# Kernel tuning notes

Hardware: AMD Instinct MI355X
Metric: run time of the kernel (lower is better)

Reference implementation:

```python
import jax, jax.numpy as jnp
import numpy as np

N_NODES = 50000
N_EDGES = 800000
IN_DIM = 256
HIDDEN = 32
HEADS = 4
OUT_DIM = 64


def setup_inputs() -> dict:
    key = jax.random.key(0)
    k1, k2, k3, k4, k5, k6, k7 = jax.random.split(key, 7)
    h = jax.random.normal(k1, (N_NODES, IN_DIM), dtype=jnp.float32)
    src = jax.random.randint(k2, (N_EDGES,), 0, N_NODES, dtype=jnp.int32)
    dst = jax.random.randint(k3, (N_EDGES,), 0, N_NODES, dtype=jnp.int32)
    # xavier_normal with relu gain, per-head weights
    gain = float(np.sqrt(2.0))
    W1 = gain * jnp.sqrt(2.0 / (IN_DIM + HIDDEN)) * jax.random.normal(k4, (HEADS, IN_DIM, HIDDEN), dtype=jnp.float32)
    a1 = gain * jnp.sqrt(2.0 / (2 * HIDDEN + 1)) * jax.random.normal(k5, (HEADS, 2 * HIDDEN), dtype=jnp.float32)
    W2 = gain * jnp.sqrt(2.0 / (HIDDEN * HEADS + OUT_DIM)) * jax.random.normal(k6, (1, HIDDEN * HEADS, OUT_DIM), dtype=jnp.float32)
    a2 = gain * jnp.sqrt(2.0 / (2 * OUT_DIM + 1)) * jax.random.normal(k7, (1, 2 * OUT_DIM), dtype=jnp.float32)
    return {"h": h, "src": src, "dst": dst, "W1": W1, "a1": a1, "W2": W2, "a2": a2}


def _gat_layer(x, src, dst, W, a):
    # x: [N, in], W: [H, in, d], a: [H, 2d]
    N = x.shape[0]
    d = W.shape[-1]
    z = jnp.einsum('ni,hio->nho', x, W)                    # [N, H, d]
    a_s, a_d = a[:, :d], a[:, d:]
    es = jnp.einsum('nho,ho->nh', z, a_s)                  # per-node src score
    ed = jnp.einsum('nho,ho->nh', z, a_d)                  # per-node dst score
    e = jax.nn.leaky_relu(es[src] + ed[dst])               # [E, H]
    # segment (per-destination) softmax over incoming edges
    emax = jax.ops.segment_max(e, dst, num_segments=N)     # [N, H]
    ex = jnp.exp(e - emax[dst])
    denom = jax.ops.segment_sum(ex, dst, num_segments=N)   # [N, H]
    alpha = ex / denom[dst]                                # [E, H]
    # scatter weighted sum of source feats back to destinations
    out = jax.ops.segment_sum(alpha[:, :, None] * z[src], dst, num_segments=N)  # [N, H, d]
    return out.reshape(N, -1)


def reference(h, src, dst, W1, a1, W2, a2):
    h1 = jax.nn.elu(_gat_layer(h, src, dst, W1, a1))       # [N, HEADS*HIDDEN]
    return _gat_layer(h1, src, dst, W2, a2)                # [N, OUT_DIM]
```

## Files before the change

kernel.cpp:

```cpp
#include <hip/hip_runtime.h>
#include <hip/hip_bf16.h>
#include <math.h>

#define N_NODES 50000
#define N_EDGES 800000
#define IN_DIM 256
#define HID 32
#define HEADS 4
#define OUT_DIM 64

#define SCAN_CHUNK 1024
#define SCAN_BLOCKS ((N_NODES + SCAN_CHUNK - 1) / SCAN_CHUNK)

typedef __attribute__((ext_vector_type(8))) short bf16x8;
typedef __attribute__((ext_vector_type(4))) float f32x4;

__device__ __forceinline__ float lrelu(float e) { return e > 0.f ? e : 0.01f * e; }
__device__ __forceinline__ float bflo(unsigned u) { return __uint_as_float(u << 16); }
__device__ __forceinline__ float bfhi(unsigned u) { return __uint_as_float(u & 0xffff0000u); }

__device__ __forceinline__ unsigned short rne_bf16(float x) {
    unsigned u = __float_as_uint(x);
    unsigned r = u + 0x7fffu + ((u >> 16) & 1u);
    return (unsigned short)(r >> 16);
}

__device__ __forceinline__ void splitf(float x, short& hi, short& lo) {
    unsigned u = __float_as_uint(x);
    unsigned short h = (unsigned short)(u >> 16);
    float hf = __uint_as_float(((unsigned)h) << 16);
    float l = x - hf;
    unsigned short lb = (unsigned short)(__float_as_uint(l) >> 16);
    hi = (short)h;
    lo = (short)lb;
}


__global__ void __launch_bounds__(256) prep_kernel(
        const float* __restrict__ W1, const float* __restrict__ a1,
        const float* __restrict__ W2, const float* __restrict__ a2,
        unsigned short* __restrict__ B1h, unsigned short* __restrict__ B1l,
        unsigned short* __restrict__ B2h, unsigned short* __restrict__ B2l,
        int* __restrict__ count) {
    int gid = blockIdx.x * 256 + threadIdx.x;
    if (gid < N_NODES) count[gid] = 0;

    int k = blockIdx.x;
    int c = threadIdx.x;
    if (c < 144) {
        float val = 0.f;
        if (c < 128) {
            val = W1[(size_t)(c >> 5) * IN_DIM * HID + (size_t)k * HID + (c & 31)];
        } else if (c < 136) {
            int j = c - 128;
            int hd = (j < 4) ? j : (j - 4);
            int off = (j < 4) ? 0 : HID;
            const float* Wp = W1 + (size_t)hd * IN_DIM * HID + (size_t)k * HID;
            const float* ap = a1 + hd * 2 * HID + off;
            float s = 0.f;
            for (int o = 0; o < HID; o++) s += Wp[o] * ap[o];
            val = s;
        }
        unsigned short hi = rne_bf16(val);
        float hf = __uint_as_float(((unsigned)hi) << 16);
        unsigned short lo = rne_bf16(val - hf);
        int s_ = k >> 5, q = (k >> 3) & 3, j8 = k & 7;
        int nt = c >> 4, L = q * 16 + (c & 15);
        size_t idx = (((size_t)s_ * 9 + nt) * 64 + L) * 8 + j8;
        B1h[idx] = hi;
        B1l[idx] = lo;
    } else if (c >= 160 && c < 240 && k < 128) {
        int c2 = c - 160;
        float val = 0.f;
        if (c2 < 64) {
            val = W2[(size_t)k * OUT_DIM + c2];
        } else if (c2 < 66) {
            const float* ap = a2 + (c2 - 64) * OUT_DIM;
            const float* Wp = W2 + (size_t)k * OUT_DIM;
            float s = 0.f;
            for (int o = 0; o < OUT_DIM; o++) s += Wp[o] * ap[o];
            val = s;
        }
        unsigned short hi = rne_bf16(val);
        float hf = __uint_as_float(((unsigned)hi) << 16);
        unsigned short lo = rne_bf16(val - hf);
        int s_ = k >> 5, q = (k >> 3) & 3, j8 = k & 7;
        int nt = c2 >> 4, L = q * 16 + (c2 & 15);
        size_t idx = (((size_t)s_ * 5 + nt) * 64 + L) * 8 + j8;
        B2h[idx] = hi;
        B2l[idx] = lo;
    }
}


__global__ void hist_kernel(const int* __restrict__ dst, int* __restrict__ count,
                            int* __restrict__ rank) {
    int i = blockIdx.x * blockDim.x + threadIdx.x;
    if (i < N_EDGES) rank[i] = atomicAdd(&count[dst[i]], 1);
}

__global__ void scan1_kernel(const int* __restrict__ count, int* __restrict__ row_start,
                             int* __restrict__ blocksum) {
    __shared__ int sdata[256];
    int t = threadIdx.x;
    int base = blockIdx.x * SCAN_CHUNK + t * 4;
    int v[4];
    int s = 0;
#pragma unroll
    for (int j = 0; j < 4; j++) {
        int idx = base + j;
        int x = (idx < N_NODES) ? count[idx] : 0;
        v[j] = x;
        s += x;
    }
    sdata[t] = s;
    __syncthreads();
    for (int off = 1; off < 256; off <<= 1) {
        int u = (t >= off) ? sdata[t - off] : 0;
        __syncthreads();
        sdata[t] += u;
        __syncthreads();
    }
    int excl = sdata[t] - s;
#pragma unroll
    for (int j = 0; j < 4; j++) {
        int idx = base + j;
        if (idx < N_NODES) row_start[idx] = excl;
        excl += v[j];
    }
    if (t == 255) blocksum[blockIdx.x] = sdata[255];
}

__global__ void scan23_kernel(int* __restrict__ row_start, const int* __restrict__ blocksum) {
    __shared__ int pre;
    int t = threadIdx.x;
    if (t < 64) {
        int v = (t < SCAN_BLOCKS) ? blocksum[t] : 0;
#pragma unroll
        for (int off = 1; off < 64; off <<= 1) {
            int u = __shfl_up(v, off);
            if (t >= off) v += u;
        }
        if (t == blockIdx.x) pre = v - blocksum[t];
    }
    __syncthreads();
    int add = pre;
    int base = blockIdx.x * SCAN_CHUNK + t * 4;
#pragma unroll
    for (int j = 0; j < 4; j++) {
        int idx = base + j;
        if (idx < N_NODES) row_start[idx] += add;
    }
}

__global__ void scatter_kernel(const int* __restrict__ src, const int* __restrict__ dst,
                               const int* __restrict__ rank, const int* __restrict__ row_start,
                               int* __restrict__ esrc) {
    int i = blockIdx.x * blockDim.x + threadIdx.x;
    if (i < N_EDGES) esrc[row_start[dst[i]] + rank[i]] = src[i];
}


__global__ void __launch_bounds__(256) proj1_mfma(
        const float* __restrict__ h, const unsigned short* __restrict__ Bh,
        const unsigned short* __restrict__ Bl, __hip_bfloat16* __restrict__ z1b,
        float* __restrict__ es1, float* __restrict__ ed1) {
    int tid = threadIdx.x;
    int wave = tid >> 6;
    int L = tid & 63;
    int q = L >> 4, L15 = L & 15;
    int n0 = blockIdx.x * 64 + wave * 16;

    int rowA = n0 + L15;
    int rrA = rowA < N_NODES ? rowA : N_NODES - 1;
    const float* hrow = h + (size_t)rrA * IN_DIM + q * 8;

    f32x4 acc[9];
#pragma unroll
    for (int nt = 0; nt < 9; nt++) acc[nt] = (f32x4)(0.f);

    float4 x0 = *(const float4*)(hrow);
    float4 x1 = *(const float4*)(hrow + 4);

#pragma unroll
    for (int s = 0; s < 8; s++) {
        int sn = (s < 7) ? s + 1 : 7;
        float4 p0 = *(const float4*)(hrow + sn * 32);
        float4 p1 = *(const float4*)(hrow + sn * 32 + 4);

        float xs[8] = {x0.x, x0.y, x0.z, x0.w, x1.x, x1.y, x1.z, x1.w};
        bf16x8 ah, al;
#pragma unroll
        for (int j = 0; j < 8; j++) {
            short hi, lo;
            splitf(xs[j], hi, lo);
            ah[j] = hi;
            al[j] = lo;
        }

        const bf16x8* bhp = (const bf16x8*)(Bh + ((size_t)s * 9 * 64) * 8 + (size_t)L * 8);
        const bf16x8* blp = (const bf16x8*)(Bl + ((size_t)s * 9 * 64) * 8 + (size_t)L * 8);
#pragma unroll
        for (int nt = 0; nt < 9; nt++) {
            bf16x8 bh = bhp[nt * 64];
            acc[nt] = __builtin_amdgcn_mfma_f32_16x16x32_bf16(ah, bh, acc[nt], 0, 0, 0);
            acc[nt] = __builtin_amdgcn_mfma_f32_16x16x32_bf16(al, bh, acc[nt], 0, 0, 0);
        }
        {
            bf16x8 bl8 = blp[8 * 64];
            acc[8] = __builtin_amdgcn_mfma_f32_16x16x32_bf16(ah, bl8, acc[8], 0, 0, 0);
        }
        x0 = p0;
        x1 = p1;
    }

#pragma unroll
    for (int r = 0; r < 4; r++) {
        int rowc = n0 + q * 4 + r;
        if (rowc < N_NODES) {
#pragma unroll
            for (int nt = 0; nt < 8; nt++)
                z1b[(size_t)rowc * 128 + nt * 16 + L15] = __float2bfloat16(acc[nt][r]);
            if (L15 < 4) es1[rowc * HEADS + L15] = acc[8][r];
            else if (L15 < 8) ed1[rowc * HEADS + (L15 - 4)] = acc[8][r];
        }
    }
}


__global__ void __launch_bounds__(256) agg1_kernel(
        const __hip_bfloat16* __restrict__ z1b, const float* __restrict__ es1,
        const float* __restrict__ ed1, const int* __restrict__ row_start,
        const int* __restrict__ count, const int* __restrict__ esrc,
        __hip_bfloat16* __restrict__ h1b) {
    int v = blockIdx.x * 4 + (threadIdx.x >> 6);
    int L = threadIdx.x & 63;
    int sub = L >> 4;
    int c16 = L & 15;
    int hd = c16 >> 2;
    int beg = row_start[v], deg = count[v];
    float edv = ed1[v * HEADS + hd];
    const int* ep = esrc + beg;
    float lacc = 0.f;
    float acc[8];
#pragma unroll
    for (int i = 0; i < 8; i++) acc[i] = 0.f;
    const uint4* zq = (const uint4*)z1b;

    for (int j0 = 0; j0 < deg; j0 += 32) {
        int se[8];
        uint4 u[8];
        float ev[8];
#pragma unroll
        for (int g = 0; g < 8; g++) {
            if (j0 + g * 4 < deg) {
                int e = j0 + g * 4 + sub;
                se[g] = ep[(e < deg) ? e : 0];
            }
        }
#pragma unroll
        for (int g = 0; g < 8; g++) {
            if (j0 + g * 4 < deg) {
                u[g] = zq[(size_t)se[g] * 16 + c16];
                ev[g] = es1[se[g] * HEADS + hd];
            }
        }
#pragma unroll
        for (int g = 0; g < 8; g++) {
            if (j0 + g * 4 < deg) {
                bool val = (j0 + g * 4 + sub) < deg;
                float q = val ? __expf(lrelu(ev[g] + edv)) : 0.f;
                lacc += q;
                acc[0] = fmaf(q, bflo(u[g].x), acc[0]);
                acc[1] = fmaf(q, bfhi(u[g].x), acc[1]);
                acc[2] = fmaf(q, bflo(u[g].y), acc[2]);
                acc[3] = fmaf(q, bfhi(u[g].y), acc[3]);
                acc[4] = fmaf(q, bflo(u[g].z), acc[4]);
                acc[5] = fmaf(q, bfhi(u[g].z), acc[5]);
                acc[6] = fmaf(q, bflo(u[g].w), acc[6]);
                acc[7] = fmaf(q, bfhi(u[g].w), acc[7]);
            }
        }
    }
    lacc += __shfl_xor(lacc, 1);
    lacc += __shfl_xor(lacc, 2);
    lacc += __shfl_xor(lacc, 16);
    lacc += __shfl_xor(lacc, 32);
    lacc *= 0.25f;
#pragma unroll
    for (int i = 0; i < 8; i++) {
        acc[i] += __shfl_xor(acc[i], 16);
        acc[i] += __shfl_xor(acc[i], 32);
    }
    if (L < 16) {
        float inv = (deg > 0) ? 1.f / lacc : 0.f;
        unsigned w[4];
#pragma unroll
        for (int i = 0; i < 4; i++) {
            float r0 = acc[2 * i] * inv;
            float r1 = acc[2 * i + 1] * inv;
            r0 = r0 > 0.f ? r0 : __expf(r0) - 1.f;
            r1 = r1 > 0.f ? r1 : __expf(r1) - 1.f;
            w[i] = (unsigned)rne_bf16(r0) | ((unsigned)rne_bf16(r1) << 16);
        }
        uint4* dst = (uint4*)(h1b + (size_t)v * 128 + c16 * 8);
        *dst = make_uint4(w[0], w[1], w[2], w[3]);
    }
}


__global__ void __launch_bounds__(256) proj2_mfma(
        const __hip_bfloat16* __restrict__ h1b, const unsigned short* __restrict__ Bh,
        const unsigned short* __restrict__ Bl, __hip_bfloat16* __restrict__ z2b,
        float* __restrict__ es2, float* __restrict__ ed2) {
    int tid = threadIdx.x;
    int wave = tid >> 6;
    int L = tid & 63;
    int q = L >> 4, L15 = L & 15;
    int n0 = blockIdx.x * 64 + wave * 16;

    int rowA = n0 + L15;
    int rrA = rowA < N_NODES ? rowA : N_NODES - 1;
    const bf16x8* hq = (const bf16x8*)(h1b + (size_t)rrA * 128);

    f32x4 acc[5];
#pragma unroll
    for (int nt = 0; nt < 5; nt++) acc[nt] = (f32x4)(0.f);

#pragma unroll
    for (int s = 0; s < 4; s++) {
        bf16x8 a = hq[s * 4 + q];
        const bf16x8* bhp = (const bf16x8*)(Bh + ((size_t)s * 5 * 64) * 8 + (size_t)L * 8);
        const bf16x8* blp = (const bf16x8*)(Bl + ((size_t)s * 5 * 64) * 8 + (size_t)L * 8);
#pragma unroll
        for (int nt = 0; nt < 5; nt++)
            acc[nt] = __builtin_amdgcn_mfma_f32_16x16x32_bf16(a, bhp[nt * 64], acc[nt], 0, 0, 0);
        acc[4] = __builtin_amdgcn_mfma_f32_16x16x32_bf16(a, blp[4 * 64], acc[4], 0, 0, 0);
    }

#pragma unroll
    for (int r = 0; r < 4; r++) {
        int rowc = n0 + q * 4 + r;
        if (rowc < N_NODES) {
#pragma unroll
            for (int nt = 0; nt < 4; nt++)
                z2b[(size_t)rowc * OUT_DIM + nt * 16 + L15] = __float2bfloat16(acc[nt][r]);
            if (L15 == 0) es2[rowc] = acc[4][r];
            else if (L15 == 1) ed2[rowc] = acc[4][r];
        }
    }
}


__global__ void __launch_bounds__(256) agg2_kernel(
        const __hip_bfloat16* __restrict__ z2b, const float* __restrict__ es2,
        const float* __restrict__ ed2, const int* __restrict__ row_start,
        const int* __restrict__ count, const int* __restrict__ esrc,
        float* __restrict__ out) {
    int v = blockIdx.x * 4 + (threadIdx.x >> 6);
    int L = threadIdx.x & 63;
    int sub = L >> 3;
    int c8 = L & 7;
    int beg = row_start[v], deg = count[v];
    float edv = ed2[v];
    const int* ep = esrc + beg;
    float lacc = 0.f;
    float acc[8];
#pragma unroll
    for (int i = 0; i < 8; i++) acc[i] = 0.f;
    const uint4* zq = (const uint4*)z2b;

    for (int j0 = 0; j0 < deg; j0 += 32) {
        int se[4];
        uint4 u[4];
        float ev[4];
#pragma unroll
        for (int g = 0; g < 4; g++) {
            if (j0 + g * 8 < deg) {
                int e = j0 + g * 8 + sub;
                se[g] = ep[(e < deg) ? e : 0];
            }
        }
#pragma unroll
        for (int g = 0; g < 4; g++) {
            if (j0 + g * 8 < deg) {
                u[g] = zq[(size_t)se[g] * 8 + c8];
                ev[g] = es2[se[g]];
            }
        }
#pragma unroll
        for (int g = 0; g < 4; g++) {
            if (j0 + g * 8 < deg) {
                bool val = (j0 + g * 8 + sub) < deg;
                float q = val ? __expf(lrelu(ev[g] + edv)) : 0.f;
                lacc += q;
                acc[0] = fmaf(q, bflo(u[g].x), acc[0]);
                acc[1] = fmaf(q, bfhi(u[g].x), acc[1]);
                acc[2] = fmaf(q, bflo(u[g].y), acc[2]);
                acc[3] = fmaf(q, bfhi(u[g].y), acc[3]);
                acc[4] = fmaf(q, bflo(u[g].z), acc[4]);
                acc[5] = fmaf(q, bfhi(u[g].z), acc[5]);
                acc[6] = fmaf(q, bflo(u[g].w), acc[6]);
                acc[7] = fmaf(q, bfhi(u[g].w), acc[7]);
            }
        }
    }
    lacc += __shfl_xor(lacc, 8);
    lacc += __shfl_xor(lacc, 16);
    lacc += __shfl_xor(lacc, 32);
#pragma unroll
    for (int i = 0; i < 8; i++) {
        acc[i] += __shfl_xor(acc[i], 8);
        acc[i] += __shfl_xor(acc[i], 16);
        acc[i] += __shfl_xor(acc[i], 32);
    }
    if (L < 8) {
        float inv = (deg > 0) ? 1.f / lacc : 0.f;
        float4 r0, r1;
#pragma unroll
        for (int i = 0; i < 8; i++) {
            float r = acc[i] * inv;
            if (i < 4) (&r0.x)[i] = r;
            else (&r1.x)[i - 4] = r;
        }
        float* dst = out + (size_t)v * OUT_DIM + c8 * 8;
        *(float4*)dst = r0;
        *(float4*)(dst + 4) = r1;
    }
}


extern "C" void kernel_launch(void* const* d_in, const int* in_sizes, int n_in,
                              void* d_out, int out_size, void* d_ws, size_t ws_size,
                              hipStream_t stream) {
    const float* h  = (const float*)d_in[0];
    const int* src  = (const int*)d_in[1];
    const int* dst  = (const int*)d_in[2];
    const float* W1 = (const float*)d_in[3];
    const float* a1 = (const float*)d_in[4];
    const float* W2 = (const float*)d_in[5];
    const float* a2 = (const float*)d_in[6];
    float* out = (float*)d_out;

    char* w = (char*)d_ws;
    size_t off = 0;
    auto alloc = [&](size_t bytes) {
        void* p = w + off;
        off = (off + bytes + 255) & ~(size_t)255;
        return p;
    };
    __hip_bfloat16* z1b = (__hip_bfloat16*)alloc((size_t)N_NODES * 128 * 2);
    float* es1 = (float*)alloc((size_t)N_NODES * HEADS * 4);
    float* ed1 = (float*)alloc((size_t)N_NODES * HEADS * 4);
    __hip_bfloat16* h1b = (__hip_bfloat16*)alloc((size_t)N_NODES * 128 * 2);
    __hip_bfloat16* z2b = (__hip_bfloat16*)alloc((size_t)N_NODES * OUT_DIM * 2);
    float* es2 = (float*)alloc((size_t)N_NODES * 4);
    float* ed2 = (float*)alloc((size_t)N_NODES * 4);
    int* count     = (int*)alloc((size_t)N_NODES * 4);
    int* row_start = (int*)alloc((size_t)N_NODES * 4);
    int* rank      = (int*)alloc((size_t)N_EDGES * 4);
    int* blocksum  = (int*)alloc((size_t)SCAN_BLOCKS * 4);
    int* esrc      = (int*)alloc((size_t)N_EDGES * 4);
    unsigned short* Bf1h = (unsigned short*)alloc((size_t)8 * 9 * 64 * 8 * 2);
    unsigned short* Bf1l = (unsigned short*)alloc((size_t)8 * 9 * 64 * 8 * 2);
    unsigned short* Bf2h = (unsigned short*)alloc((size_t)4 * 5 * 64 * 8 * 2);
    unsigned short* Bf2l = (unsigned short*)alloc((size_t)4 * 5 * 64 * 8 * 2);

    prep_kernel<<<256, 256, 0, stream>>>(W1, a1, W2, a2, Bf1h, Bf1l, Bf2h, Bf2l, count);
    hist_kernel<<<(N_EDGES + 255) / 256, 256, 0, stream>>>(dst, count, rank);
    scan1_kernel<<<SCAN_BLOCKS, 256, 0, stream>>>(count, row_start, blocksum);
    scan23_kernel<<<SCAN_BLOCKS, 256, 0, stream>>>(row_start, blocksum);
    scatter_kernel<<<(N_EDGES + 255) / 256, 256, 0, stream>>>(src, dst, rank, row_start, esrc);

    const int MBLK = (N_NODES + 63) / 64;
    proj1_mfma<<<MBLK, 256, 0, stream>>>(h, Bf1h, Bf1l, z1b, es1, ed1);
    agg1_kernel<<<N_NODES / 4, 256, 0, stream>>>(z1b, es1, ed1, row_start, count, esrc, h1b);
    proj2_mfma<<<MBLK, 256, 0, stream>>>(h1b, Bf2h, Bf2l, z2b, es2, ed2);
    agg2_kernel<<<N_NODES / 4, 256, 0, stream>>>(z2b, es2, ed2, row_start, count, esrc, out);
}
```

Baseline: 234.4 us.

## Fuse CSR build and layer-1 projection into one cooperative kernel

Replaces the six front-end launches (prep, histogram, two scans, scatter, proj1) with a single cooperative kernel. Half the blocks build the CSR using software grid barriers and keep dst and rank in registers, so the rank array is no longer written and reread. The other half prepare weights and then run the layer-1 MFMA projection concurrently. This removes launch gaps and overlaps the latency-bound CSR work with the compute-bound projection, at the cost of spin-wait barriers, a memset, and a fallback path if the cooperative launch fails.

```diff
diff --git a/kernel.cpp b/kernel.cpp
--- a/kernel.cpp
+++ b/kernel.cpp
@@ -11,6 +11,13 @@
 
 #define SCAN_CHUNK 1024
 #define SCAN_BLOCKS ((N_NODES + SCAN_CHUNK - 1) / SCAN_CHUNK)
+
+#define NCSR 512
+#define NPROJ 512
+#define NGRID (NCSR + NPROJ)
+#define CSR_T (NCSR * 256)
+#define EPT ((N_EDGES + CSR_T - 1) / CSR_T)
+#define NTASK ((N_NODES + 15) / 16)
 
 typedef __attribute__((ext_vector_type(8))) short bf16x8;
 typedef __attribute__((ext_vector_type(4))) float f32x4;
@@ -36,17 +43,25 @@
 }
 
 
-__global__ void __launch_bounds__(256) prep_kernel(
+__device__ __forceinline__ void bar_wait(int* ctr, int nblk) {
+    __syncthreads();
+    if (threadIdx.x == 0) {
+        __threadfence();
+        __hip_atomic_fetch_add(ctr, 1, __ATOMIC_RELEASE, __HIP_MEMORY_SCOPE_AGENT);
+        while (__hip_atomic_load(ctr, __ATOMIC_RELAXED, __HIP_MEMORY_SCOPE_AGENT) < nblk) {
+            __builtin_amdgcn_s_sleep(8);
+        }
+        __threadfence();
+    }
+    __syncthreads();
+}
+
+
+__device__ __forceinline__ void prep_body(int k, int c,
         const float* __restrict__ W1, const float* __restrict__ a1,
         const float* __restrict__ W2, const float* __restrict__ a2,
         unsigned short* __restrict__ B1h, unsigned short* __restrict__ B1l,
-        unsigned short* __restrict__ B2h, unsigned short* __restrict__ B2l,
-        int* __restrict__ count) {
-    int gid = blockIdx.x * 256 + threadIdx.x;
-    if (gid < N_NODES) count[gid] = 0;
-
-    int k = blockIdx.x;
-    int c = threadIdx.x;
+        unsigned short* __restrict__ B2h, unsigned short* __restrict__ B2l) {
     if (c < 144) {
         float val = 0.f;
         if (c < 128) {
@@ -92,18 +107,9 @@
     }
 }
 
-
-__global__ void hist_kernel(const int* __restrict__ dst, int* __restrict__ count,
-                            int* __restrict__ rank) {
-    int i = blockIdx.x * blockDim.x + threadIdx.x;
-    if (i < N_EDGES) rank[i] = atomicAdd(&count[dst[i]], 1);
-}
-
-__global__ void scan1_kernel(const int* __restrict__ count, int* __restrict__ row_start,
-                             int* __restrict__ blocksum) {
-    __shared__ int sdata[256];
-    int t = threadIdx.x;
-    int base = blockIdx.x * SCAN_CHUNK + t * 4;
+__device__ __forceinline__ void scan1_body(int bid, int t, const int* __restrict__ count,
+        int* __restrict__ row_start, int* __restrict__ blocksum, int* sdata) {
+    int base = bid * SCAN_CHUNK + t * 4;
     int v[4];
     int s = 0;
 #pragma unroll
@@ -128,12 +134,11 @@
         if (idx < N_NODES) row_start[idx] = excl;
         excl += v[j];
     }
-    if (t == 255) blocksum[blockIdx.x] = sdata[255];
-}
-
-__global__ void scan23_kernel(int* __restrict__ row_start, const int* __restrict__ blocksum) {
-    __shared__ int pre;
-    int t = threadIdx.x;
+    if (t == 255) blocksum[bid] = sdata[255];
+}
+
+__device__ __forceinline__ void scan23_body(int bid, int t, int* __restrict__ row_start,
+        const int* __restrict__ blocksum, int* pre) {
     if (t < 64) {
         int v = (t < SCAN_BLOCKS) ? blocksum[t] : 0;
 #pragma unroll
@@ -141,16 +146,156 @@
             int u = __shfl_up(v, off);
             if (t >= off) v += u;
         }
-        if (t == blockIdx.x) pre = v - blocksum[t];
+        if (t == bid) *pre = v - blocksum[t];
     }
     __syncthreads();
-    int add = pre;
-    int base = blockIdx.x * SCAN_CHUNK + t * 4;
+    int add = *pre;
+    int base = bid * SCAN_CHUNK + t * 4;
 #pragma unroll
     for (int j = 0; j < 4; j++) {
         int idx = base + j;
         if (idx < N_NODES) row_start[idx] += add;
     }
+}
+
+__device__ __forceinline__ void proj1_body(int n0, int L,
+        const float* __restrict__ h, const unsigned short* __restrict__ Bh,
+        const unsigned short* __restrict__ Bl, __hip_bfloat16* __restrict__ z1b,
+        float* __restrict__ es1, float* __restrict__ ed1) {
+    int q = L >> 4, L15 = L & 15;
+    int rowA = n0 + L15;
+    int rrA = rowA < N_NODES ? rowA : N_NODES - 1;
+    const float* hrow = h + (size_t)rrA * IN_DIM + q * 8;
+
+    f32x4 acc[9];
+#pragma unroll
+    for (int nt = 0; nt < 9; nt++) acc[nt] = (f32x4)(0.f);
+
+    float4 x0 = *(const float4*)(hrow);
+    float4 x1 = *(const float4*)(hrow + 4);
+
+#pragma unroll
+    for (int s = 0; s < 8; s++) {
+        int sn = (s < 7) ? s + 1 : 7;
+        float4 p0 = *(const float4*)(hrow + sn * 32);
+        float4 p1 = *(const float4*)(hrow + sn * 32 + 4);
+
+        float xs[8] = {x0.x, x0.y, x0.z, x0.w, x1.x, x1.y, x1.z, x1.w};
+        bf16x8 ah, al;
+#pragma unroll
+        for (int j = 0; j < 8; j++) {
+            short hi, lo;
+            splitf(xs[j], hi, lo);
+            ah[j] = hi;
+            al[j] = lo;
+        }
+
+        const bf16x8* bhp = (const bf16x8*)(Bh + ((size_t)s * 9 * 64) * 8 + (size_t)L * 8);
+        const bf16x8* blp = (const bf16x8*)(Bl + ((size_t)s * 9 * 64) * 8 + (size_t)L * 8);
+#pragma unroll
+        for (int nt = 0; nt < 9; nt++) {
+            bf16x8 bh = bhp[nt * 64];
+            acc[nt] = __builtin_amdgcn_mfma_f32_16x16x32_bf16(ah, bh, acc[nt], 0, 0, 0);
+            acc[nt] = __builtin_amdgcn_mfma_f32_16x16x32_bf16(al, bh, acc[nt], 0, 0, 0);
+        }
+        {
+            bf16x8 bl8 = blp[8 * 64];
+            acc[8] = __builtin_amdgcn_mfma_f32_16x16x32_bf16(ah, bl8, acc[8], 0, 0, 0);
+        }
+        x0 = p0;
+        x1 = p1;
+    }
+
+#pragma unroll
+    for (int r = 0; r < 4; r++) {
+        int rowc = n0 + q * 4 + r;
+        if (rowc < N_NODES) {
+#pragma unroll
+            for (int nt = 0; nt < 8; nt++)
+                z1b[(size_t)rowc * 128 + nt * 16 + L15] = __float2bfloat16(acc[nt][r]);
+            if (L15 < 4) es1[rowc * HEADS + L15] = acc[8][r];
+            else if (L15 < 8) ed1[rowc * HEADS + (L15 - 4)] = acc[8][r];
+        }
+    }
+}
+
+
+__global__ void __launch_bounds__(256, 4) fused_front(
+        const float* __restrict__ h, const float* __restrict__ W1,
+        const float* __restrict__ a1, const float* __restrict__ W2,
+        const float* __restrict__ a2,
+        unsigned short* __restrict__ B1h, unsigned short* __restrict__ B1l,
+        unsigned short* __restrict__ B2h, unsigned short* __restrict__ B2l,
+        const int* __restrict__ src, const int* __restrict__ dst,
+        int* __restrict__ count, int* __restrict__ row_start,
+        int* __restrict__ blocksum, int* __restrict__ esrc,
+        __hip_bfloat16* __restrict__ z1b, float* __restrict__ es1,
+        float* __restrict__ ed1, int* __restrict__ bars) {
+    __shared__ int sdata[256];
+    __shared__ int pre;
+    int bid = blockIdx.x;
+    int t = threadIdx.x;
+
+    if (bid < NCSR) {
+        int gid = bid * 256 + t;
+        if (gid < N_NODES) atomicExch(&count[gid], 0);
+        bar_wait(&bars[0], NCSR);
+        int dv[EPT], rv[EPT];
+#pragma unroll
+        for (int k = 0; k < EPT; k++) {
+            int e = gid + k * CSR_T;
+            if (e < N_EDGES) {
+                dv[k] = dst[e];
+                rv[k] = atomicAdd(&count[dv[k]], 1);
+            }
+        }
+        bar_wait(&bars[1], NCSR);
+        if (bid < SCAN_BLOCKS) scan1_body(bid, t, count, row_start, blocksum, sdata);
+        bar_wait(&bars[2], NCSR);
+        if (bid < SCAN_BLOCKS) scan23_body(bid, t, row_start, blocksum, &pre);
+        bar_wait(&bars[3], NCSR);
+#pragma unroll
+        for (int k = 0; k < EPT; k++) {
+            int e = gid + k * CSR_T;
+            if (e < N_EDGES) esrc[row_start[dv[k]] + rv[k]] = src[e];
+        }
+    } else {
+        int k = bid - NCSR;
+        if (k < 256) prep_body(k, t, W1, a1, W2, a2, B1h, B1l, B2h, B2l);
+        bar_wait(&bars[4], NPROJ);
+        int wave = t >> 6, L = t & 63;
+        for (int task = k * 4 + wave; task < NTASK; task += NPROJ * 4)
+            proj1_body(task * 16, L, h, B1h, B1l, z1b, es1, ed1);
+    }
+}
+
+
+__global__ void __launch_bounds__(256) prep_kernel(
+        const float* __restrict__ W1, const float* __restrict__ a1,
+        const float* __restrict__ W2, const float* __restrict__ a2,
+        unsigned short* __restrict__ B1h, unsigned short* __restrict__ B1l,
+        unsigned short* __restrict__ B2h, unsigned short* __restrict__ B2l,
+        int* __restrict__ count) {
+    int gid = blockIdx.x * 256 + threadIdx.x;
+    if (gid < N_NODES) count[gid] = 0;
+    prep_body(blockIdx.x, threadIdx.x, W1, a1, W2, a2, B1h, B1l, B2h, B2l);
+}
+
+__global__ void hist_kernel(const int* __restrict__ dst, int* __restrict__ count,
+                            int* __restrict__ rank) {
+    int i = blockIdx.x * blockDim.x + threadIdx.x;
+    if (i < N_EDGES) rank[i] = atomicAdd(&count[dst[i]], 1);
+}
+
+__global__ void scan1_kernel(const int* __restrict__ count, int* __restrict__ row_start,
+                             int* __restrict__ blocksum) {
+    __shared__ int sdata[256];
+    scan1_body(blockIdx.x, threadIdx.x, count, row_start, blocksum, sdata);
+}
+
+__global__ void scan23_kernel(int* __restrict__ row_start, const int* __restrict__ blocksum) {
+    __shared__ int pre;
+    scan23_body(blockIdx.x, threadIdx.x, row_start, blocksum, &pre);
 }
 
 __global__ void scatter_kernel(const int* __restrict__ src, const int* __restrict__ dst,
@@ -159,7 +304,6 @@
     int i = blockIdx.x * blockDim.x + threadIdx.x;
     if (i < N_EDGES) esrc[row_start[dst[i]] + rank[i]] = src[i];
 }
-
 
 __global__ void __launch_bounds__(256) proj1_mfma(
         const float* __restrict__ h, const unsigned short* __restrict__ Bh,
@@ -168,63 +312,8 @@
     int tid = threadIdx.x;
     int wave = tid >> 6;
     int L = tid & 63;
-    int q = L >> 4, L15 = L & 15;
     int n0 = blockIdx.x * 64 + wave * 16;
-
-    int rowA = n0 + L15;
-    int rrA = rowA < N_NODES ? rowA : N_NODES - 1;
-    const float* hrow = h + (size_t)rrA * IN_DIM + q * 8;
-
-    f32x4 acc[9];
-#pragma unroll
-    for (int nt = 0; nt < 9; nt++) acc[nt] = (f32x4)(0.f);
-
-    float4 x0 = *(const float4*)(hrow);
-    float4 x1 = *(const float4*)(hrow + 4);
-
-#pragma unroll
-    for (int s = 0; s < 8; s++) {
-        int sn = (s < 7) ? s + 1 : 7;
-        float4 p0 = *(const float4*)(hrow + sn * 32);
-        float4 p1 = *(const float4*)(hrow + sn * 32 + 4);
-
-        float xs[8] = {x0.x, x0.y, x0.z, x0.w, x1.x, x1.y, x1.z, x1.w};
-        bf16x8 ah, al;
-#pragma unroll
-        for (int j = 0; j < 8; j++) {
-            short hi, lo;
-            splitf(xs[j], hi, lo);
-            ah[j] = hi;
-            al[j] = lo;
-        }
-
-        const bf16x8* bhp = (const bf16x8*)(Bh + ((size_t)s * 9 * 64) * 8 + (size_t)L * 8);
-        const bf16x8* blp = (const bf16x8*)(Bl + ((size_t)s * 9 * 64) * 8 + (size_t)L * 8);
-#pragma unroll
-        for (int nt = 0; nt < 9; nt++) {
-            bf16x8 bh = bhp[nt * 64];
-            acc[nt] = __builtin_amdgcn_mfma_f32_16x16x32_bf16(ah, bh, acc[nt], 0, 0, 0);
-            acc[nt] = __builtin_amdgcn_mfma_f32_16x16x32_bf16(al, bh, acc[nt], 0, 0, 0);
-        }
-        {
-            bf16x8 bl8 = blp[8 * 64];
-            acc[8] = __builtin_amdgcn_mfma_f32_16x16x32_bf16(ah, bl8, acc[8], 0, 0, 0);
-        }
-        x0 = p0;
-        x1 = p1;
-    }
-
-#pragma unroll
-    for (int r = 0; r < 4; r++) {
-        int rowc = n0 + q * 4 + r;
-        if (rowc < N_NODES) {
-#pragma unroll
-            for (int nt = 0; nt < 8; nt++)
-                z1b[(size_t)rowc * 128 + nt * 16 + L15] = __float2bfloat16(acc[nt][r]);
-            if (L15 < 4) es1[rowc * HEADS + L15] = acc[8][r];
-            else if (L15 < 8) ed1[rowc * HEADS + (L15 - 4)] = acc[8][r];
-        }
-    }
+    proj1_body(n0, L, h, Bh, Bl, z1b, es1, ed1);
 }
 
 
@@ -303,8 +392,8 @@
             r1 = r1 > 0.f ? r1 : __expf(r1) - 1.f;
             w[i] = (unsigned)rne_bf16(r0) | ((unsigned)rne_bf16(r1) << 16);
         }
-        uint4* dst = (uint4*)(h1b + (size_t)v * 128 + c16 * 8);
-        *dst = make_uint4(w[0], w[1], w[2], w[3]);
+        uint4* dstp = (uint4*)(h1b + (size_t)v * 128 + c16 * 8);
+        *dstp = make_uint4(w[0], w[1], w[2], w[3]);
     }
 }
 
@@ -423,9 +512,9 @@
             if (i < 4) (&r0.x)[i] = r;
             else (&r1.x)[i - 4] = r;
         }
-        float* dst = out + (size_t)v * OUT_DIM + c8 * 8;
-        *(float4*)dst = r0;
-        *(float4*)(dst + 4) = r1;
+        float* dstp = out + (size_t)v * OUT_DIM + c8 * 8;
+        *(float4*)dstp = r0;
+        *(float4*)(dstp + 4) = r1;
     }
 }
 
@@ -465,15 +554,29 @@
     unsigned short* Bf1l = (unsigned short*)alloc((size_t)8 * 9 * 64 * 8 * 2);
     unsigned short* Bf2h = (unsigned short*)alloc((size_t)4 * 5 * 64 * 8 * 2);
     unsigned short* Bf2l = (unsigned short*)alloc((size_t)4 * 5 * 64 * 8 * 2);
-
-    prep_kernel<<<256, 256, 0, stream>>>(W1, a1, W2, a2, Bf1h, Bf1l, Bf2h, Bf2l, count);
-    hist_kernel<<<(N_EDGES + 255) / 256, 256, 0, stream>>>(dst, count, rank);
-    scan1_kernel<<<SCAN_BLOCKS, 256, 0, stream>>>(count, row_start, blocksum);
-    scan23_kernel<<<SCAN_BLOCKS, 256, 0, stream>>>(row_start, blocksum);
-    scatter_kernel<<<(N_EDGES + 255) / 256, 256, 0, stream>>>(src, dst, rank, row_start, esrc);
+    int* bars = (int*)alloc(8 * sizeof(int));
 
     const int MBLK = (N_NODES + 63) / 64;
-    proj1_mfma<<<MBLK, 256, 0, stream>>>(h, Bf1h, Bf1l, z1b, es1, ed1);
+
+    hipMemsetAsync(bars, 0, 8 * sizeof(int), stream);
+
+    void* kargs[] = {(void*)&h, (void*)&W1, (void*)&a1, (void*)&W2, (void*)&a2,
+                     (void*)&Bf1h, (void*)&Bf1l, (void*)&Bf2h, (void*)&Bf2l,
+                     (void*)&src, (void*)&dst, (void*)&count, (void*)&row_start,
+                     (void*)&blocksum, (void*)&esrc, (void*)&z1b, (void*)&es1,
+                     (void*)&ed1, (void*)&bars};
+    hipError_t ce = hipLaunchCooperativeKernel(
+        reinterpret_cast<const void*>(&fused_front), dim3(NGRID), dim3(256),
+        kargs, 0, stream);
+    if (ce != hipSuccess) {
+        prep_kernel<<<256, 256, 0, stream>>>(W1, a1, W2, a2, Bf1h, Bf1l, Bf2h, Bf2l, count);
+        hist_kernel<<<(N_EDGES + 255) / 256, 256, 0, stream>>>(dst, count, rank);
+        scan1_kernel<<<SCAN_BLOCKS, 256, 0, stream>>>(count, row_start, blocksum);
+        scan23_kernel<<<SCAN_BLOCKS, 256, 0, stream>>>(row_start, blocksum);
+        scatter_kernel<<<(N_EDGES + 255) / 256, 256, 0, stream>>>(src, dst, rank, row_start, esrc);
+        proj1_mfma<<<MBLK, 256, 0, stream>>>(h, Bf1h, Bf1l, z1b, es1, ed1);
+    }
+
     agg1_kernel<<<N_NODES / 4, 256, 0, stream>>>(z1b, es1, ed1, row_start, count, esrc, h1b);
     proj2_mfma<<<MBLK, 256, 0, stream>>>(h1b, Bf2h, Bf2l, z2b, es2, ed2);
     agg2_kernel<<<N_NODES / 4, 256, 0, stream>>>(z2b, es2, ed2, row_start, count, esrc, out);
```

After: 629.3 us. 168% more time.

## Fuse prep with histogram and single-block scan with proj1 to cut launches

Applied to the files above, without the earlier changes.

Merges the weight prep kernel and the edge histogram into one launch, replaces the three-kernel multi-block scan with a single-block scan, and runs that scan as block 0 of the layer-1 projection kernel. Count zeroing moves to a memset. The goal is fewer kernel launches and dependency bubbles, and letting the scan overlap with the projection. The cost is a serial scan in one block where each thread loops over about 196 strided elements with uncoalesced loads, which may end up on the critical path before scatter.

```diff
diff --git a/kernel.cpp b/kernel.cpp
--- a/kernel.cpp
+++ b/kernel.cpp
@@ -9,8 +9,8 @@
 #define HEADS 4
 #define OUT_DIM 64
 
-#define SCAN_CHUNK 1024
-#define SCAN_BLOCKS ((N_NODES + SCAN_CHUNK - 1) / SCAN_CHUNK)
+#define HIST_BLOCKS ((N_EDGES + 255) / 256)
+#define MBLK ((N_NODES + 63) / 64)
 
 typedef __attribute__((ext_vector_type(8))) short bf16x8;
 typedef __attribute__((ext_vector_type(4))) float f32x4;
@@ -36,17 +36,11 @@
 }
 
 
-__global__ void __launch_bounds__(256) prep_kernel(
+__device__ __forceinline__ void prep_body(int k, int c,
         const float* __restrict__ W1, const float* __restrict__ a1,
         const float* __restrict__ W2, const float* __restrict__ a2,
         unsigned short* __restrict__ B1h, unsigned short* __restrict__ B1l,
-        unsigned short* __restrict__ B2h, unsigned short* __restrict__ B2l,
-        int* __restrict__ count) {
-    int gid = blockIdx.x * 256 + threadIdx.x;
-    if (gid < N_NODES) count[gid] = 0;
-
-    int k = blockIdx.x;
-    int c = threadIdx.x;
+        unsigned short* __restrict__ B2h, unsigned short* __restrict__ B2l) {
     if (c < 144) {
         float val = 0.f;
         if (c < 128) {
@@ -93,25 +87,32 @@
 }
 
 
-__global__ void hist_kernel(const int* __restrict__ dst, int* __restrict__ count,
-                            int* __restrict__ rank) {
-    int i = blockIdx.x * blockDim.x + threadIdx.x;
-    if (i < N_EDGES) rank[i] = atomicAdd(&count[dst[i]], 1);
-}
-
-__global__ void scan1_kernel(const int* __restrict__ count, int* __restrict__ row_start,
-                             int* __restrict__ blocksum) {
+__global__ void __launch_bounds__(256) prep_hist_kernel(
+        const float* __restrict__ W1, const float* __restrict__ a1,
+        const float* __restrict__ W2, const float* __restrict__ a2,
+        unsigned short* __restrict__ B1h, unsigned short* __restrict__ B1l,
+        unsigned short* __restrict__ B2h, unsigned short* __restrict__ B2l,
+        const int* __restrict__ dst, int* __restrict__ count,
+        int* __restrict__ rank) {
+    int bid = blockIdx.x;
+    if (bid < 256) {
+        prep_body(bid, threadIdx.x, W1, a1, W2, a2, B1h, B1l, B2h, B2l);
+    } else {
+        int i = (bid - 256) * 256 + threadIdx.x;
+        if (i < N_EDGES) rank[i] = atomicAdd(&count[dst[i]], 1);
+    }
+}
+
+
+__device__ __forceinline__ void scan_block_body(const int* __restrict__ count,
+                                                int* __restrict__ row_start, int t) {
     __shared__ int sdata[256];
-    int t = threadIdx.x;
-    int base = blockIdx.x * SCAN_CHUNK + t * 4;
-    int v[4];
+    const int PER = (N_NODES + 255) / 256;
+    int base = t * PER;
     int s = 0;
-#pragma unroll
-    for (int j = 0; j < 4; j++) {
+    for (int j = 0; j < PER; j++) {
         int idx = base + j;
-        int x = (idx < N_NODES) ? count[idx] : 0;
-        v[j] = x;
-        s += x;
+        if (idx < N_NODES) s += count[idx];
     }
     sdata[t] = s;
     __syncthreads();
@@ -122,109 +123,99 @@
         __syncthreads();
     }
     int excl = sdata[t] - s;
-#pragma unroll
-    for (int j = 0; j < 4; j++) {
+    for (int j = 0; j < PER; j++) {
         int idx = base + j;
-        if (idx < N_NODES) row_start[idx] = excl;
-        excl += v[j];
-    }
-    if (t == 255) blocksum[blockIdx.x] = sdata[255];
-}
-
-__global__ void scan23_kernel(int* __restrict__ row_start, const int* __restrict__ blocksum) {
-    __shared__ int pre;
-    int t = threadIdx.x;
-    if (t < 64) {
-        int v = (t < SCAN_BLOCKS) ? blocksum[t] : 0;
-#pragma unroll
-        for (int off = 1; off < 64; off <<= 1) {
-            int u = __shfl_up(v, off);
-            if (t >= off) v += u;
-        }
-        if (t == blockIdx.x) pre = v - blocksum[t];
-    }
-    __syncthreads();
-    int add = pre;
-    int base = blockIdx.x * SCAN_CHUNK + t * 4;
-#pragma unroll
-    for (int j = 0; j < 4; j++) {
-        int idx = base + j;
-        if (idx < N_NODES) row_start[idx] += add;
-    }
-}
+        if (idx < N_NODES) {
+            row_start[idx] = excl;
+            excl += count[idx];
+        }
+    }
+}
+
+
+__device__ __forceinline__ void proj1_body(int n0, int L,
+        const float* __restrict__ h, const unsigned short* __restrict__ Bh,
+        const unsigned short* __restrict__ Bl, __hip_bfloat16* __restrict__ z1b,
+        float* __restrict__ es1, float* __restrict__ ed1) {
+    int q = L >> 4, L15 = L & 15;
+    int rowA = n0 + L15;
+    int rrA = rowA < N_NODES ? rowA : N_NODES - 1;
+    const float* hrow = h + (size_t)rrA * IN_DIM + q * 8;
+
+    f32x4 acc[9];
+#pragma unroll
+    for (int nt = 0; nt < 9; nt++) acc[nt] = (f32x4)(0.f);
+
+    float4 x0 = *(const float4*)(hrow);
+    float4 x1 = *(const float4*)(hrow + 4);
+
+#pragma unroll
+    for (int s = 0; s < 8; s++) {
+        int sn = (s < 7) ? s + 1 : 7;
+        float4 p0 = *(const float4*)(hrow + sn * 32);
+        float4 p1 = *(const float4*)(hrow + sn * 32 + 4);
+
+        float xs[8] = {x0.x, x0.y, x0.z, x0.w, x1.x, x1.y, x1.z, x1.w};
+        bf16x8 ah, al;
+#pragma unroll
+        for (int j = 0; j < 8; j++) {
+            short hi, lo;
+            splitf(xs[j], hi, lo);
+            ah[j] = hi;
+            al[j] = lo;
+        }
+
+        const bf16x8* bhp = (const bf16x8*)(Bh + ((size_t)s * 9 * 64) * 8 + (size_t)L * 8);
+        const bf16x8* blp = (const bf16x8*)(Bl + ((size_t)s * 9 * 64) * 8 + (size_t)L * 8);
+#pragma unroll
+        for (int nt = 0; nt < 9; nt++) {
+            bf16x8 bh = bhp[nt * 64];
+            acc[nt] = __builtin_amdgcn_mfma_f32_16x16x32_bf16(ah, bh, acc[nt], 0, 0, 0);
+            acc[nt] = __builtin_amdgcn_mfma_f32_16x16x32_bf16(al, bh, acc[nt], 0, 0, 0);
+        }
+        {
+            bf16x8 bl8 = blp[8 * 64];
+            acc[8] = __builtin_amdgcn_mfma_f32_16x16x32_bf16(ah, bl8, acc[8], 0, 0, 0);
+        }
+        x0 = p0;
+        x1 = p1;
+    }
+
+#pragma unroll
+    for (int r = 0; r < 4; r++) {
+        int rowc = n0 + q * 4 + r;
+        if (rowc < N_NODES) {
+#pragma unroll
+            for (int nt = 0; nt < 8; nt++)
+                z1b[(size_t)rowc * 128 + nt * 16 + L15] = __float2bfloat16(acc[nt][r]);
+            if (L15 < 4) es1[rowc * HEADS + L15] = acc[8][r];
+            else if (L15 < 8) ed1[rowc * HEADS + (L15 - 4)] = acc[8][r];
+        }
+    }
+}
+
+
+__global__ void __launch_bounds__(256) scan_proj1_kernel(
+        const float* __restrict__ h, const unsigned short* __restrict__ Bh,
+        const unsigned short* __restrict__ Bl, __hip_bfloat16* __restrict__ z1b,
+        float* __restrict__ es1, float* __restrict__ ed1,
+        const int* __restrict__ count, int* __restrict__ row_start) {
+    if (blockIdx.x == 0) {
+        scan_block_body(count, row_start, threadIdx.x);
+        return;
+    }
+    int wave = threadIdx.x >> 6;
+    int L = threadIdx.x & 63;
+    int n0 = (blockIdx.x - 1) * 64 + wave * 16;
+    proj1_body(n0, L, h, Bh, Bl, z1b, es1, ed1);
+}
+
 
 __global__ void scatter_kernel(const int* __restrict__ src, const int* __restrict__ dst,
                                const int* __restrict__ rank, const int* __restrict__ row_start,
                                int* __restrict__ esrc) {
     int i = blockIdx.x * blockDim.x + threadIdx.x;
     if (i < N_EDGES) esrc[row_start[dst[i]] + rank[i]] = src[i];
-}
-
-
-__global__ void __launch_bounds__(256) proj1_mfma(
-        const float* __restrict__ h, const unsigned short* __restrict__ Bh,
-        const unsigned short* __restrict__ Bl, __hip_bfloat16* __restrict__ z1b,
-        float* __restrict__ es1, float* __restrict__ ed1) {
-    int tid = threadIdx.x;
-    int wave = tid >> 6;
-    int L = tid & 63;
-    int q = L >> 4, L15 = L & 15;
-    int n0 = blockIdx.x * 64 + wave * 16;
-
-    int rowA = n0 + L15;
-    int rrA = rowA < N_NODES ? rowA : N_NODES - 1;
-    const float* hrow = h + (size_t)rrA * IN_DIM + q * 8;
-
-    f32x4 acc[9];
-#pragma unroll
-    for (int nt = 0; nt < 9; nt++) acc[nt] = (f32x4)(0.f);
-
-    float4 x0 = *(const float4*)(hrow);
-    float4 x1 = *(const float4*)(hrow + 4);
-
-#pragma unroll
-    for (int s = 0; s < 8; s++) {
-        int sn = (s < 7) ? s + 1 : 7;
-        float4 p0 = *(const float4*)(hrow + sn * 32);
-        float4 p1 = *(const float4*)(hrow + sn * 32 + 4);
-
-        float xs[8] = {x0.x, x0.y, x0.z, x0.w, x1.x, x1.y, x1.z, x1.w};
-        bf16x8 ah, al;
-#pragma unroll
-        for (int j = 0; j < 8; j++) {
-            short hi, lo;
-            splitf(xs[j], hi, lo);
-            ah[j] = hi;
-            al[j] = lo;
-        }
-
-        const bf16x8* bhp = (const bf16x8*)(Bh + ((size_t)s * 9 * 64) * 8 + (size_t)L * 8);
-        const bf16x8* blp = (const bf16x8*)(Bl + ((size_t)s * 9 * 64) * 8 + (size_t)L * 8);
-#pragma unroll
-        for (int nt = 0; nt < 9; nt++) {
-            bf16x8 bh = bhp[nt * 64];
-            acc[nt] = __builtin_amdgcn_mfma_f32_16x16x32_bf16(ah, bh, acc[nt], 0, 0, 0);
-            acc[nt] = __builtin_amdgcn_mfma_f32_16x16x32_bf16(al, bh, acc[nt], 0, 0, 0);
-        }
-        {
-            bf16x8 bl8 = blp[8 * 64];
-            acc[8] = __builtin_amdgcn_mfma_f32_16x16x32_bf16(ah, bl8, acc[8], 0, 0, 0);
-        }
-        x0 = p0;
-        x1 = p1;
-    }
-
-#pragma unroll
-    for (int r = 0; r < 4; r++) {
-        int rowc = n0 + q * 4 + r;
-        if (rowc < N_NODES) {
-#pragma unroll
-            for (int nt = 0; nt < 8; nt++)
-                z1b[(size_t)rowc * 128 + nt * 16 + L15] = __float2bfloat16(acc[nt][r]);
-            if (L15 < 4) es1[rowc * HEADS + L15] = acc[8][r];
-            else if (L15 < 8) ed1[rowc * HEADS + (L15 - 4)] = acc[8][r];
-        }
-    }
 }
 
 
@@ -303,8 +294,8 @@
             r1 = r1 > 0.f ? r1 : __expf(r1) - 1.f;
             w[i] = (unsigned)rne_bf16(r0) | ((unsigned)rne_bf16(r1) << 16);
         }
-        uint4* dst = (uint4*)(h1b + (size_t)v * 128 + c16 * 8);
-        *dst = make_uint4(w[0], w[1], w[2], w[3]);
+        uint4* dstp = (uint4*)(h1b + (size_t)v * 128 + c16 * 8);
+        *dstp = make_uint4(w[0], w[1], w[2], w[3]);
     }
 }
 
@@ -423,9 +414,9 @@
             if (i < 4) (&r0.x)[i] = r;
             else (&r1.x)[i - 4] = r;
         }
-        float* dst = out + (size_t)v * OUT_DIM + c8 * 8;
-        *(float4*)dst = r0;
-        *(float4*)(dst + 4) = r1;
+        float* dstp = out + (size_t)v * OUT_DIM + c8 * 8;
+        *(float4*)dstp = r0;
+        *(float4*)(dstp + 4) = r1;
     }
 }
 
@@ -459,21 +450,22 @@
     int* count     = (int*)alloc((size_t)N_NODES * 4);
     int* row_start = (int*)alloc((size_t)N_NODES * 4);
     int* rank      = (int*)alloc((size_t)N_EDGES * 4);
-    int* blocksum  = (int*)alloc((size_t)SCAN_BLOCKS * 4);
     int* esrc      = (int*)alloc((size_t)N_EDGES * 4);
     unsigned short* Bf1h = (unsigned short*)alloc((size_t)8 * 9 * 64 * 8 * 2);
     unsigned short* Bf1l = (unsigned short*)alloc((size_t)8 * 9 * 64 * 8 * 2);
     unsigned short* Bf2h = (unsigned short*)alloc((size_t)4 * 5 * 64 * 8 * 2);
     unsigned short* Bf2l = (unsigned short*)alloc((size_t)4 * 5 * 64 * 8 * 2);
 
-    prep_kernel<<<256, 256, 0, stream>>>(W1, a1, W2, a2, Bf1h, Bf1l, Bf2h, Bf2l, count);
-    hist_kernel<<<(N_EDGES + 255) / 256, 256, 0, stream>>>(dst, count, rank);
-    scan1_kernel<<<SCAN_BLOCKS, 256, 0, stream>>>(count, row_start, blocksum);
-    scan23_kernel<<<SCAN_BLOCKS, 256, 0, stream>>>(row_start, blocksum);
-    scatter_kernel<<<(N_EDGES + 255) / 256, 256, 0, stream>>>(src, dst, rank, row_start, esrc);
-
-    const int MBLK = (N_NODES + 63) / 64;
-    proj1_mfma<<<MBLK, 256, 0, stream>>>(h, Bf1h, Bf1l, z1b, es1, ed1);
+    hipMemsetAsync(count, 0, (size_t)N_NODES * 4, stream);
+
+    prep_hist_kernel<<<256 + HIST_BLOCKS, 256, 0, stream>>>(
+        W1, a1, W2, a2, Bf1h, Bf1l, Bf2h, Bf2l, dst, count, rank);
+
+    scan_proj1_kernel<<<1 + MBLK, 256, 0, stream>>>(
+        h, Bf1h, Bf1l, z1b, es1, ed1, count, row_start);
+
+    scatter_kernel<<<HIST_BLOCKS, 256, 0, stream>>>(src, dst, rank, row_start, esrc);
+
     agg1_kernel<<<N_NODES / 4, 256, 0, stream>>>(z1b, es1, ed1, row_start, count, esrc, h1b);
     proj2_mfma<<<MBLK, 256, 0, stream>>>(h1b, Bf2h, Bf2l, z2b, es2, ed2);
     agg2_kernel<<<N_NODES / 4, 256, 0, stream>>>(z2b, es2, ed2, row_start, count, esrc, out);
```

Result: slower. 317.7 us (+35.5%).
